# Performance work log

Measured on AMD Instinct MI355X. Metric: run time of the kernel, lower is better.

The kernel has to match this reference:

```python
import jax, jax.numpy as jnp
import numpy as np

N, R, M, E, NE, B = 50000, 500, 120000, 960000, 800000, 8192
D, H1, HID, OC = 200, 256, 512, 50


def setup_inputs() -> dict:
    key = jax.random.key(0)
    ks = jax.random.split(key, 26)
    s = 0.05
    rn = lambda k, shp: jax.random.normal(k, shp, jnp.float32) * s
    return {
        "entity_emb": jax.random.normal(ks[0], (N, D), jnp.float32),
        "rel_emb": jax.random.normal(ks[1], (R, D), jnp.float32),
        "b_x": jax.random.randint(ks[2], (M,), 0, N),
        "b_node_graph_index": jax.random.randint(ks[3], (M,), 0, R),
        "edge_src": jax.random.randint(ks[4], (E,), 0, M),
        "edge_dst": jax.random.randint(ks[5], (E,), 0, M),
        "edge_w": jax.random.uniform(ks[6], (E,), jnp.float32),
        "big_src": jax.random.randint(ks[7], (NE,), 0, N),
        "big_dst": jax.random.randint(ks[8], (NE,), 0, N),
        "big_w": jax.random.uniform(ks[9], (NE,), jnp.float32),
        "perm": jax.random.permutation(ks[10], N),
        "batch_inputs": jnp.stack([
            jax.random.randint(ks[11], (B,), 0, N),
            jax.random.randint(ks[12], (B,), 0, R),
            jax.random.randint(ks[13], (B,), 0, N)], axis=1),
        "W1a": rn(ks[14], (2 * D, H1)), "W1b": rn(ks[15], (H1, D)),
        "W2a": rn(ks[16], (D, H1)), "W2b": rn(ks[17], (H1, D)),
        "Wle": rn(ks[18], (2 * D, 1)), "ble": jnp.zeros((1,), jnp.float32),
        "Wlo": rn(ks[19], (2 * D, D)), "blo": jnp.zeros((D,), jnp.float32),
        "Wg": rn(ks[20], (D, HID)), "Wd": rn(ks[21], (HID, HID)),
        "conv_w": rn(ks[22], (OC, 3)), "conv_b": jnp.zeros((OC,), jnp.float32),
        "fc_w": rn(ks[23], (OC * D, 1)), "fc_b": jnp.zeros((1,), jnp.float32),
    }


def _l2norm(x):
    return x / jnp.maximum(jnp.linalg.norm(x, axis=-1, keepdims=True), 1e-12)


def _gcn(x, src, dst, w, n, Wa, Wb):
    # two-layer GCN over sparse edge list: out = A @ relu(A @ x @ Wa) @ Wb
    agg = lambda h: jax.ops.segment_sum(h[src] * w[:, None], dst, num_segments=n)
    h = jax.nn.relu(agg(x) @ Wa)
    return agg(h) @ Wb


def _seg_softmax(v, idx, n):
    m = jax.ops.segment_max(v, idx, num_segments=n)
    e = jnp.exp(v - m[idx])
    s = jax.ops.segment_sum(e, idx, num_segments=n)
    return e / (s[idx] + 1e-16)


def _mce(ent, rel, b_x, b_gi, src, dst, w, W1a, W1b, Wle, ble, Wlo, blo):
    x = jnp.concatenate([ent[b_x], rel[b_gi]], axis=-1)          # [M, 400]
    e = _gcn(x, src, dst, w, b_x.shape[0], W1a, W1b)             # [M, 200]
    cnt = jax.ops.segment_sum(jnp.ones((b_x.shape[0],), e.dtype), b_x, num_segments=N)
    mean = jax.ops.segment_sum(e, b_x, num_segments=N) / jnp.maximum(cnt, 1.0)[:, None]
    z = mean[b_x]                                                # scatter_mean then gather
    emb = jnp.concatenate([e[b_x], z], axis=-1)                  # [M, 400]
    score = emb @ Wle + ble                                      # [M, 1]
    zs = _seg_softmax(score, b_x, N)                             # segment softmax
    pooled = jax.ops.segment_sum(zs * emb, b_x, num_segments=N)  # [N, 400]
    return (pooled @ Wlo + blo) + ent


def _dgi(h1, h2, Wg, Wd):
    p1 = jax.nn.relu(h1 @ Wg)
    p2 = jax.nn.relu(h2 @ Wg)
    c = jax.nn.sigmoid(jnp.mean(p1, axis=0))                     # readout [HID]
    t = Wd @ c
    return jnp.concatenate([p1 @ t, p2 @ t])                     # [2N]


def _convkb(trip, conv_w, conv_b, fc_w, fc_b):
    # trip [B,3,D]; Conv2d(1, OC, (1,3)) over [B,1,D,3] -> [B,OC,D]
    h = jax.nn.relu(jnp.einsum('bsd,os->bod', trip, conv_w) + conv_b[None, :, None])
    return h.reshape(trip.shape[0], -1) @ fc_w + fc_b            # [B,1]


def reference(entity_emb, rel_emb, b_x, b_node_graph_index, edge_src, edge_dst,
              edge_w, big_src, big_dst, big_w, perm, batch_inputs,
              W1a, W1b, W2a, W2b, Wle, ble, Wlo, blo, Wg, Wd,
              conv_w, conv_b, fc_w, fc_b):
    ent = _l2norm(entity_emb)
    rel = _l2norm(rel_emb)
    ent_shuf = ent[perm]
    ec = _mce(ent, rel, b_x, b_node_graph_index, edge_src, edge_dst, edge_w,
              W1a, W1b, Wle, ble, Wlo, blo)
    ec_ = _mce(ent_shuf, rel, b_x, b_node_graph_index, edge_src, edge_dst, edge_w,
               W1a, W1b, Wle, ble, Wlo, blo)
    eg = _gcn(ec, big_src, big_dst, big_w, N, W2a, W2b)
    eg_ = _gcn(ec_, big_src, big_dst, big_w, N, W2a, W2b)
    local_logits = _dgi(ec, ec_, Wg, Wd)
    global_logits = _dgi(eg, eg_, Wg, Wd)
    trip = jnp.stack([ec[batch_inputs[:, 0]], rel[batch_inputs[:, 1]],
                      ec[batch_inputs[:, 2]]], axis=1)           # [B,3,D]
    out_conv = _convkb(trip, conv_w, conv_b, fc_w, fc_b)
    return out_conv, local_logits, global_logits
```

## Files before the change

kernel.cpp:

```cpp
#include <hip/hip_runtime.h>

#define NN   50000
#define RR   500
#define MM   120000
#define EE   960000
#define NEE  800000
#define BB   8192
#define DD   200
#define HH1  256
#define HIDD 512
#define OCC  50

typedef unsigned int  u32;
typedef unsigned short u16;
typedef __attribute__((ext_vector_type(8))) short bf16x8;
typedef __attribute__((ext_vector_type(4))) float f32x4;

static __device__ __forceinline__ float bf2f(u16 u) {
    u32 x = ((u32)u) << 16;
    return __uint_as_float(x);
}
static __device__ __forceinline__ u16 f2bf(float f) {
    u32 x = __float_as_uint(f);
    u32 r = (x + 0x7FFFu + ((x >> 16) & 1u)) >> 16;
    return (u16)r;
}
static __device__ __forceinline__ u32 pack2(float a, float b) {
    return (u32)f2bf(a) | ((u32)f2bf(b) << 16);
}
static __device__ __forceinline__ void unpack2(u32 v, float& a, float& b) {
    a = bf2f((u16)(v & 0xFFFFu));
    b = bf2f((u16)(v >> 16));
}

static __device__ __forceinline__ float wredsum(float v) {
#pragma unroll
    for (int off = 32; off > 0; off >>= 1) v += __shfl_xor(v, off);
    return v;
}

template<typename T> static __device__ __forceinline__ void stv(T* p, size_t i, float v);
template<> __device__ __forceinline__ void stv<float>(float* p, size_t i, float v) { p[i] = v; }
template<> __device__ __forceinline__ void stv<u16>(u16* p, size_t i, float v) { p[i] = f2bf(v); }

static __device__ __forceinline__ u32 relu2bf(u32 x) {
    if (x & 0x00008000u) x &= 0xFFFF0000u;
    if (x & 0x80000000u) x &= 0x0000FFFFu;
    return x;
}

__global__ void k_l2norm(const float* __restrict__ in, float* __restrict__ outf,
                         u16* __restrict__ outb, int rows) {
    int w = (blockIdx.x * blockDim.x + threadIdx.x) >> 6;
    int lane = threadIdx.x & 63;
    if (w >= rows) return;
    const float* r = in + (size_t)w * DD;
    float s = 0.f;
    for (int d = lane; d < DD; d += 64) { float v = r[d]; s += v * v; }
    s = wredsum(s);
    float inv = 1.0f / fmaxf(sqrtf(s), 1e-12f);
    for (int d = lane; d < DD; d += 64) {
        float v = r[d] * inv;
        if (outf) outf[(size_t)w * DD + d] = v;
        if (outb) outb[(size_t)w * DD + d] = f2bf(v);
    }
}

__global__ void k_gather_perm(const int* __restrict__ bx, const int* __restrict__ perm,
                              int* __restrict__ idx1, int M) {
    int m = blockIdx.x * blockDim.x + threadIdx.x;
    if (m < M) idx1[m] = perm[bx[m]];
}

__global__ void k_edge_idx(const int* __restrict__ srcE, const int* __restrict__ map,
                           int* __restrict__ outE, int n) {
    int e = blockIdx.x * blockDim.x + threadIdx.x;
    if (e < n) outE[e] = map[srcE[e]];
}

__global__ void k_hist(const int* __restrict__ idx, int* __restrict__ cnt, int n) {
    int i = blockIdx.x * blockDim.x + threadIdx.x;
    if (i < n) atomicAdd(&cnt[idx[i]], 1);
}

__global__ __launch_bounds__(1024) void k_scan(const int* __restrict__ in,
                                               int* __restrict__ out, int n) {
    __shared__ int wtot[16];
    __shared__ int wexc[16];
    __shared__ int s_carry;
    int tid = threadIdx.x, lane = tid & 63, wid = tid >> 6;
    if (tid == 0) s_carry = 0;
    __syncthreads();
    for (int base = 0; base < n; base += 1024) {
        int i = base + tid;
        int v = (i < n) ? in[i] : 0;
        int x = v;
#pragma unroll
        for (int off = 1; off < 64; off <<= 1) {
            int t = __shfl_up(x, off);
            if (lane >= off) x += t;
        }
        if (lane == 63) wtot[wid] = x;
        __syncthreads();
        if (wid == 0) {
            int wv2 = (lane < 16) ? wtot[lane] : 0;
            int y = wv2;
#pragma unroll
            for (int off = 1; off < 16; off <<= 1) {
                int t = __shfl_up(y, off);
                if (lane >= off) y += t;
            }
            if (lane < 16) wexc[lane] = y - wv2;
            if (lane == 15) wtot[15] = y;
        }
        __syncthreads();
        if (i < n) out[i] = s_carry + wexc[wid] + (x - v);
        int chunk_total = wtot[15];
        __syncthreads();
        if (tid == 0) s_carry += chunk_total;
        __syncthreads();
    }
    if (threadIdx.x == 0) out[n] = s_carry;
}

__global__ void k_fill2(const int* __restrict__ dst, const int* __restrict__ src,
                        const float* __restrict__ w, int* __restrict__ cursor,
                        int* __restrict__ srcs_out, float* __restrict__ ws_out, int n) {
    int e = blockIdx.x * blockDim.x + threadIdx.x;
    if (e >= n) return;
    int p = atomicAdd(&cursor[dst[e]], 1);
    srcs_out[p] = src[e];
    ws_out[p] = w[e];
}

__global__ void k_fill1(const int* __restrict__ idx, int* __restrict__ cursor,
                        int* __restrict__ outm, int n) {
    int m = blockIdx.x * blockDim.x + threadIdx.x;
    if (m >= n) return;
    int p = atomicAdd(&cursor[idx[m]], 1);
    outm[p] = m;
}

__global__ void k_pull_mce(const int* __restrict__ rp, const int* __restrict__ ivE,
                           const int* __restrict__ giE, const float* __restrict__ wE,
                           const u16* __restrict__ Pent, const u16* __restrict__ Prel,
                           u16* __restrict__ out, int ndst) {
    int wv = (blockIdx.x * blockDim.x + threadIdx.x) >> 6;
    if (wv >= ndst) return;
    int lane = threadIdx.x & 63;
    int beg = rp[wv], end = rp[wv + 1];
    float accA[2] = {0.f, 0.f}, accB[2] = {0.f, 0.f};
    int e = beg;
    for (; e + 4 <= end; e += 4) {
        int i0 = ivE[e], i1 = ivE[e + 1], i2 = ivE[e + 2], i3 = ivE[e + 3];
        int g0 = giE[e], g1 = giE[e + 1], g2 = giE[e + 2], g3 = giE[e + 3];
        float w0 = wE[e], w1 = wE[e + 1], w2 = wE[e + 2], w3 = wE[e + 3];
        const u32* pe0 = (const u32*)(Pent + (size_t)i0 * HH1);
        const u32* pe1 = (const u32*)(Pent + (size_t)i1 * HH1);
        const u32* pe2 = (const u32*)(Pent + (size_t)i2 * HH1);
        const u32* pe3 = (const u32*)(Pent + (size_t)i3 * HH1);
        const u32* pr0 = (const u32*)(Prel + (size_t)g0 * HH1);
        const u32* pr1 = (const u32*)(Prel + (size_t)g1 * HH1);
        const u32* pr2 = (const u32*)(Prel + (size_t)g2 * HH1);
        const u32* pr3 = (const u32*)(Prel + (size_t)g3 * HH1);
        u32 vp[4][2], vr[4][2];
#pragma unroll
        for (int t = 0; t < 2; ++t) {
            int p = lane + 64 * t;
            vp[0][t] = pe0[p]; vp[1][t] = pe1[p]; vp[2][t] = pe2[p]; vp[3][t] = pe3[p];
            vr[0][t] = pr0[p]; vr[1][t] = pr1[p]; vr[2][t] = pr2[p]; vr[3][t] = pr3[p];
        }
#pragma unroll
        for (int t = 0; t < 2; ++t) {
            float a, b, c, d;
            unpack2(vp[0][t], a, b); unpack2(vr[0][t], c, d);
            accA[t] += (a + c) * w0; accB[t] += (b + d) * w0;
            unpack2(vp[1][t], a, b); unpack2(vr[1][t], c, d);
            accA[t] += (a + c) * w1; accB[t] += (b + d) * w1;
            unpack2(vp[2][t], a, b); unpack2(vr[2][t], c, d);
            accA[t] += (a + c) * w2; accB[t] += (b + d) * w2;
            unpack2(vp[3][t], a, b); unpack2(vr[3][t], c, d);
            accA[t] += (a + c) * w3; accB[t] += (b + d) * w3;
        }
    }
    for (; e < end; ++e) {
        int iv = ivE[e], gi = giE[e];
        float w = wE[e];
        const u32* pe = (const u32*)(Pent + (size_t)iv * HH1);
        const u32* pr = (const u32*)(Prel + (size_t)gi * HH1);
#pragma unroll
        for (int t = 0; t < 2; ++t) {
            int p = lane + 64 * t;
            float a, b, c, d;
            unpack2(pe[p], a, b); unpack2(pr[p], c, d);
            accA[t] += (a + c) * w; accB[t] += (b + d) * w;
        }
    }
    u32* o = (u32*)(out + (size_t)wv * HH1);
#pragma unroll
    for (int t = 0; t < 2; ++t) o[lane + 64 * t] = pack2(accA[t], accB[t]);
}

template<int DIMS, typename TIN, typename TOUT>
__global__ void k_pull(const int* __restrict__ rp, const int* __restrict__ srcs,
                       const float* __restrict__ wsrt, const TIN* __restrict__ in,
                       TOUT* __restrict__ out, int ndst) {
    int wv = (blockIdx.x * blockDim.x + threadIdx.x) >> 6;
    if (wv >= ndst) return;
    int lane = threadIdx.x & 63;
    int beg = rp[wv], end = rp[wv + 1];
    constexpr int NP = DIMS / 2;
    constexpr int NT = (NP + 63) / 64;
    float accA[NT], accB[NT];
#pragma unroll
    for (int t = 0; t < NT; ++t) { accA[t] = 0.f; accB[t] = 0.f; }
    int e = beg;
    for (; e + 4 <= end; e += 4) {
        int s0 = srcs[e], s1 = srcs[e + 1], s2 = srcs[e + 2], s3 = srcs[e + 3];
        float w0 = wsrt[e], w1 = wsrt[e + 1], w2 = wsrt[e + 2], w3 = wsrt[e + 3];
        if constexpr (sizeof(TIN) == 2) {
            const u32* r0 = (const u32*)((const u16*)in + (size_t)s0 * DIMS);
            const u32* r1 = (const u32*)((const u16*)in + (size_t)s1 * DIMS);
            const u32* r2 = (const u32*)((const u16*)in + (size_t)s2 * DIMS);
            const u32* r3 = (const u32*)((const u16*)in + (size_t)s3 * DIMS);
            u32 v[4][NT];
#pragma unroll
            for (int t = 0; t < NT; ++t) {
                int p = lane + 64 * t;
                if (p < NP) { v[0][t] = r0[p]; v[1][t] = r1[p]; v[2][t] = r2[p]; v[3][t] = r3[p]; }
            }
#pragma unroll
            for (int t = 0; t < NT; ++t) {
                int p = lane + 64 * t;
                if (p < NP) {
                    float a, b;
                    unpack2(v[0][t], a, b); accA[t] += a * w0; accB[t] += b * w0;
                    unpack2(v[1][t], a, b); accA[t] += a * w1; accB[t] += b * w1;
                    unpack2(v[2][t], a, b); accA[t] += a * w2; accB[t] += b * w2;
                    unpack2(v[3][t], a, b); accA[t] += a * w3; accB[t] += b * w3;
                }
            }
        } else {
            const float2* r0 = (const float2*)((const float*)in + (size_t)s0 * DIMS);
            const float2* r1 = (const float2*)((const float*)in + (size_t)s1 * DIMS);
            const float2* r2 = (const float2*)((const float*)in + (size_t)s2 * DIMS);
            const float2* r3 = (const float2*)((const float*)in + (size_t)s3 * DIMS);
            float2 v[4][NT];
#pragma unroll
            for (int t = 0; t < NT; ++t) {
                int p = lane + 64 * t;
                if (p < NP) { v[0][t] = r0[p]; v[1][t] = r1[p]; v[2][t] = r2[p]; v[3][t] = r3[p]; }
            }
#pragma unroll
            for (int t = 0; t < NT; ++t) {
                int p = lane + 64 * t;
                if (p < NP) {
                    accA[t] += v[0][t].x * w0; accB[t] += v[0][t].y * w0;
                    accA[t] += v[1][t].x * w1; accB[t] += v[1][t].y * w1;
                    accA[t] += v[2][t].x * w2; accB[t] += v[2][t].y * w2;
                    accA[t] += v[3][t].x * w3; accB[t] += v[3][t].y * w3;
                }
            }
        }
    }
    for (; e < end; ++e) {
        int s = srcs[e];
        float w = wsrt[e];
        if constexpr (sizeof(TIN) == 2) {
            const u32* r = (const u32*)((const u16*)in + (size_t)s * DIMS);
#pragma unroll
            for (int t = 0; t < NT; ++t) {
                int p = lane + 64 * t;
                if (p < NP) { float a, b; unpack2(r[p], a, b); accA[t] += a * w; accB[t] += b * w; }
            }
        } else {
            const float2* r = (const float2*)((const float*)in + (size_t)s * DIMS);
#pragma unroll
            for (int t = 0; t < NT; ++t) {
                int p = lane + 64 * t;
                if (p < NP) { float2 v = r[p]; accA[t] += v.x * w; accB[t] += v.y * w; }
            }
        }
    }
    if constexpr (sizeof(TOUT) == 2) {
        u32* o = (u32*)((u16*)out + (size_t)wv * DIMS);
#pragma unroll
        for (int t = 0; t < NT; ++t) {
            int p = lane + 64 * t;
            if (p < NP) o[p] = pack2(accA[t], accB[t]);
        }
    } else {
        float2* o = (float2*)((float*)out + (size_t)wv * DIMS);
#pragma unroll
        for (int t = 0; t < NT; ++t) {
            int p = lane + 64 * t;
            if (p < NP) { float2 v; v.x = accA[t]; v.y = accB[t]; o[p] = v; }
        }
    }
}

__global__ void k_segpool(const int* __restrict__ rpX, const int* __restrict__ mids,
                          const u16* __restrict__ e_buf, u16* __restrict__ pooled, int n) {
    int nv = (blockIdx.x * blockDim.x + threadIdx.x) >> 6;
    if (nv >= n) return;
    int lane = threadIdx.x & 63;
    int beg = rpX[nv], end = rpX[nv + 1];
    int cnt = end - beg;
    float accA[2] = {0.f, 0.f}, accB[2] = {0.f, 0.f};
    int e = beg;
    for (; e + 4 <= end; e += 4) {
        const u32* r0 = (const u32*)(e_buf + (size_t)mids[e] * DD);
        const u32* r1 = (const u32*)(e_buf + (size_t)mids[e + 1] * DD);
        const u32* r2 = (const u32*)(e_buf + (size_t)mids[e + 2] * DD);
        const u32* r3 = (const u32*)(e_buf + (size_t)mids[e + 3] * DD);
        u32 v[4][2];
#pragma unroll
        for (int t = 0; t < 2; ++t) {
            int p = lane + 64 * t;
            if (p < DD / 2) { v[0][t] = r0[p]; v[1][t] = r1[p]; v[2][t] = r2[p]; v[3][t] = r3[p]; }
        }
#pragma unroll
        for (int t = 0; t < 2; ++t) {
            int p = lane + 64 * t;
            if (p < DD / 2) {
                float a, b;
                unpack2(v[0][t], a, b); accA[t] += a; accB[t] += b;
                unpack2(v[1][t], a, b); accA[t] += a; accB[t] += b;
                unpack2(v[2][t], a, b); accA[t] += a; accB[t] += b;
                unpack2(v[3][t], a, b); accA[t] += a; accB[t] += b;
            }
        }
    }
    for (; e < end; ++e) {
        const u32* r = (const u32*)(e_buf + (size_t)mids[e] * DD);
#pragma unroll
        for (int t = 0; t < 2; ++t) {
            int p = lane + 64 * t;
            if (p < DD / 2) { float a, b; unpack2(r[p], a, b); accA[t] += a; accB[t] += b; }
        }
    }
    float inv = 1.0f / fmaxf((float)cnt, 1.0f);
    bool occ = cnt > 0;
    const u32* er = (const u32*)(e_buf + (size_t)nv * DD);
    u32* p0 = (u32*)(pooled + (size_t)nv * (2 * DD));
#pragma unroll
    for (int t = 0; t < 2; ++t) {
        int p = lane + 64 * t;
        if (p < DD / 2) {
            p0[p] = occ ? er[p] : 0u;
            p0[DD / 2 + p] = occ ? pack2(accA[t] * inv, accB[t] * inv) : 0u;
        }
    }
}

template<int AMODE, int RELU_IN, int RELU_OUT, int HAS_BIAS, int HAS_ADD, int FUSE, typename TC>
__global__ __launch_bounds__(256, 2) void k_mfmamm(
    const void* __restrict__ Av, const float* __restrict__ Bw, TC* __restrict__ C,
    int Mr, int Nc, int Kd,
    const float* __restrict__ bias, const u16* __restrict__ addsrc,
    const int* __restrict__ addidx, const float* __restrict__ tvec,
    float* __restrict__ redout) {
    constexpr int BM = 128, BN = 128, BK = 32;
    constexpr int ASTR = 40;
    __shared__ u16 Ahi[BM * ASTR];
    __shared__ u16 Alo[AMODE ? (BM * ASTR) : 8];
    __shared__ u16 Bhi[BN * ASTR];
    __shared__ u16 Blo[BN * ASTR];

    int tid = threadIdx.x;
    int wid = tid >> 6, lane = tid & 63;
    int wr = wid >> 1, wc = wid & 1;
    int r = lane & 15, h = lane >> 4;
    int bm0 = blockIdx.y * BM, bn0 = blockIdx.x * BN;
    int srow = (tid & 15) + 16 * (tid >> 6);
    int sg = (tid >> 4) & 3;

    f32x4 acc[4][4];
#pragma unroll
    for (int i = 0; i < 4; ++i)
#pragma unroll
        for (int j = 0; j < 4; ++j) acc[i][j] = (f32x4){0.f, 0.f, 0.f, 0.f};

    for (int k0 = 0; k0 < Kd; k0 += BK) {
        __syncthreads();
        int kc = k0 + sg * 8;
        bool kok = (kc + 8 <= Kd);
#pragma unroll
        for (int it = 0; it < 2; ++it) {
            int row = srow + 64 * it;
            int gr = bm0 + row;
            u16* dst = Ahi + row * ASTR + sg * 8;
            if (AMODE == 0) {
                const u16* Ab = (const u16*)Av;
                uint4 v = make_uint4(0, 0, 0, 0);
                if (gr < Mr && kok) v = *(const uint4*)(Ab + (size_t)gr * Kd + kc);
                if (RELU_IN) {
                    v.x = relu2bf(v.x); v.y = relu2bf(v.y);
                    v.z = relu2bf(v.z); v.w = relu2bf(v.w);
                }
                *(uint4*)dst = v;
            } else {
                const float* Af = (const float*)Av;
                u32 hw[4] = {0, 0, 0, 0}, lw[4] = {0, 0, 0, 0};
                if (gr < Mr && kok) {
                    const float4* sp = (const float4*)(Af + (size_t)gr * Kd + kc);
                    float4 v0 = sp[0], v1 = sp[1];
                    float vs[8] = {v0.x, v0.y, v0.z, v0.w, v1.x, v1.y, v1.z, v1.w};
#pragma unroll
                    for (int qq = 0; qq < 4; ++qq) {
                        u16 h0 = f2bf(vs[2 * qq]), h1 = f2bf(vs[2 * qq + 1]);
                        hw[qq] = (u32)h0 | ((u32)h1 << 16);
                        u16 l0 = f2bf(vs[2 * qq] - bf2f(h0));
                        u16 l1 = f2bf(vs[2 * qq + 1] - bf2f(h1));
                        lw[qq] = (u32)l0 | ((u32)l1 << 16);
                    }
                }
                *(uint4*)dst = make_uint4(hw[0], hw[1], hw[2], hw[3]);
                *(uint4*)(Alo + row * ASTR + sg * 8) = make_uint4(lw[0], lw[1], lw[2], lw[3]);
            }
        }
#pragma unroll
        for (int it = 0; it < 2; ++it) {
            int n = srow + 64 * it;
            int gn = bn0 + n;
            u32 hw[4] = {0, 0, 0, 0}, lw[4] = {0, 0, 0, 0};
            if (gn < Nc) {
#pragma unroll
                for (int qq = 0; qq < 4; ++qq) {
                    int gk0 = kc + 2 * qq, gk1 = kc + 2 * qq + 1;
                    float b0 = (gk0 < Kd) ? Bw[(size_t)gk0 * Nc + gn] : 0.f;
                    float b1 = (gk1 < Kd) ? Bw[(size_t)gk1 * Nc + gn] : 0.f;
                    u16 h0 = f2bf(b0), h1 = f2bf(b1);
                    hw[qq] = (u32)h0 | ((u32)h1 << 16);
                    u16 l0 = f2bf(b0 - bf2f(h0)), l1 = f2bf(b1 - bf2f(h1));
                    lw[qq] = (u32)l0 | ((u32)l1 << 16);
                }
            }
            *(uint4*)(Bhi + n * ASTR + sg * 8) = make_uint4(hw[0], hw[1], hw[2], hw[3]);
            *(uint4*)(Blo + n * ASTR + sg * 8) = make_uint4(lw[0], lw[1], lw[2], lw[3]);
        }
        __syncthreads();
        bf16x8 af[4], al[4], bh[4], bl[4];
#pragma unroll
        for (int j = 0; j < 4; ++j) {
            int nrow = wc * 64 + j * 16 + r;
            bh[j] = *(const bf16x8*)(Bhi + nrow * ASTR + h * 8);
            bl[j] = *(const bf16x8*)(Blo + nrow * ASTR + h * 8);
        }
#pragma unroll
        for (int i = 0; i < 4; ++i) {
            int mrow = wr * 64 + i * 16 + r;
            af[i] = *(const bf16x8*)(Ahi + mrow * ASTR + h * 8);
            if (AMODE) al[i] = *(const bf16x8*)(Alo + mrow * ASTR + h * 8);
        }
#pragma unroll
        for (int i = 0; i < 4; ++i)
#pragma unroll
            for (int j = 0; j < 4; ++j) {
                acc[i][j] = __builtin_amdgcn_mfma_f32_16x16x32_bf16(af[i], bh[j], acc[i][j], 0, 0, 0);
                acc[i][j] = __builtin_amdgcn_mfma_f32_16x16x32_bf16(af[i], bl[j], acc[i][j], 0, 0, 0);
                if (AMODE)
                    acc[i][j] = __builtin_amdgcn_mfma_f32_16x16x32_bf16(al[i], bh[j], acc[i][j], 0, 0, 0);
            }
    }
    float colacc[4] = {0.f, 0.f, 0.f, 0.f};
#pragma unroll
    for (int i = 0; i < 4; ++i) {
        float rowacc[4] = {0.f, 0.f, 0.f, 0.f};
#pragma unroll
        for (int j = 0; j < 4; ++j) {
            int col = bn0 + wc * 64 + j * 16 + r;
            bool colok = col < Nc;
            float tv = (FUSE == 2 && colok) ? tvec[col] : 0.f;
#pragma unroll
            for (int rg = 0; rg < 4; ++rg) {
                int row = bm0 + wr * 64 + i * 16 + h * 4 + rg;
                float v = acc[i][j][rg];
                if (HAS_BIAS && colok) v += bias[col];
                if (RELU_OUT) v = fmaxf(v, 0.f);
                bool ok = colok && row < Mr;
                if (HAS_ADD && ok) {
                    int r2 = addidx ? addidx[row] : row;
                    v += bf2f(addsrc[(size_t)r2 * Nc + col]);
                }
                if (FUSE != 2 && ok) stv(C, (size_t)row * Nc + col, v);
                if (FUSE == 1 && ok) colacc[j] += v;
                if (FUSE == 2) rowacc[rg] += v * tv;
            }
        }
        if (FUSE == 2) {
#pragma unroll
            for (int rg = 0; rg < 4; ++rg) {
                float val = rowacc[rg];
                val += __shfl_xor(val, 1); val += __shfl_xor(val, 2);
                val += __shfl_xor(val, 4); val += __shfl_xor(val, 8);
                int row = bm0 + wr * 64 + i * 16 + h * 4 + rg;
                if (r == 0 && row < Mr) atomicAdd(&redout[row], val);
            }
        }
    }
    if (FUSE == 1) {
#pragma unroll
        for (int j = 0; j < 4; ++j) {
            float val = colacc[j];
            val += __shfl_xor(val, 16); val += __shfl_xor(val, 32);
            int col = bn0 + wc * 64 + j * 16 + r;
            if (h == 0 && col < Nc) atomicAdd(&redout[col], val);
        }
    }
}

__global__ void k_sigc(const float* __restrict__ csum, float* __restrict__ cvec) {
    int i = threadIdx.x;
    cvec[i] = 1.0f / (1.0f + expf(-csum[i] * (1.0f / (float)NN)));
}

__global__ void k_tmv(const float* __restrict__ Wd, const float* __restrict__ cvec,
                      float* __restrict__ tvec) {
    __shared__ float c[HIDD];
    int lane = threadIdx.x;
    for (int j = lane; j < HIDD; j += 64) c[j] = cvec[j];
    __syncthreads();
    int r0 = blockIdx.x * 16;
    for (int i = r0; i < r0 + 16; ++i) {
        const float* wr = Wd + (size_t)i * HIDD;
        float s = 0.f;
        for (int j = lane; j < HIDD; j += 64) s += wr[j] * c[j];
        s = wredsum(s);
        if (lane == 0) tvec[i] = s;
    }
}

__global__ void k_rowdot512(const float* __restrict__ p, const float* __restrict__ t,
                            float* __restrict__ out, int rows) {
    int g = blockIdx.x * blockDim.x + threadIdx.x;
    int wv = g >> 6;
    if (wv >= rows) return;
    int lane = g & 63;
    const float* r = p + (size_t)wv * HIDD;
    float s = 0.f;
#pragma unroll
    for (int t4 = 0; t4 < 8; ++t4) {
        int d = lane + t4 * 64;
        s += r[d] * t[d];
    }
    s = wredsum(s);
    if (lane == 0) out[wv] = s;
}

__global__ void k_convkb(const u16* __restrict__ ec, const float* __restrict__ rel,
                         const int* __restrict__ bi, const float* __restrict__ cw,
                         const float* __restrict__ cb, const float* __restrict__ fcw,
                         const float* __restrict__ fcb, float* __restrict__ out) {
    __shared__ float t0[DD], t1[DD], t2[DD];
    __shared__ float red[4];
    int b = blockIdx.x, tid = threadIdx.x;
    int i0 = bi[b * 3 + 0], i1 = bi[b * 3 + 1], i2 = bi[b * 3 + 2];
    if (tid < DD) {
        t0[tid] = bf2f(ec[(size_t)i0 * DD + tid]);
        t1[tid] = rel[(size_t)i1 * DD + tid];
        t2[tid] = bf2f(ec[(size_t)i2 * DD + tid]);
    }
    __syncthreads();
    float partial = 0.f;
    if (tid < DD) {
        float a = t0[tid], bb = t1[tid], c = t2[tid];
        for (int o = 0; o < OCC; ++o) {
            float h = fmaxf(cw[o * 3 + 0] * a + cw[o * 3 + 1] * bb + cw[o * 3 + 2] * c + cb[o], 0.f);
            partial += h * fcw[o * DD + tid];
        }
    }
    partial = wredsum(partial);
    if ((tid & 63) == 0) red[tid >> 6] = partial;
    __syncthreads();
    if (tid == 0) out[b] = red[0] + red[1] + red[2] + red[3] + fcb[0];
}

__global__ void k_sentinel(float* out, float val) { out[threadIdx.x] = val; }

extern "C" void kernel_launch(void* const* d_in, const int* in_sizes, int n_in,
                              void* d_out, int out_size, void* d_ws, size_t ws_size,
                              hipStream_t stream) {
    const float* entity_emb = (const float*)d_in[0];
    const float* rel_emb    = (const float*)d_in[1];
    const int*   b_x        = (const int*)d_in[2];
    const int*   b_gi       = (const int*)d_in[3];
    const int*   e_src      = (const int*)d_in[4];
    const int*   e_dst      = (const int*)d_in[5];
    const float* e_w        = (const float*)d_in[6];
    const int*   big_src    = (const int*)d_in[7];
    const int*   big_dst    = (const int*)d_in[8];
    const float* big_w      = (const float*)d_in[9];
    const int*   perm       = (const int*)d_in[10];
    const int*   batch_in   = (const int*)d_in[11];
    const float* W1a        = (const float*)d_in[12];
    const float* W1b        = (const float*)d_in[13];
    const float* W2a        = (const float*)d_in[14];
    const float* W2b        = (const float*)d_in[15];
    const float* Wlo        = (const float*)d_in[18];
    const float* blo        = (const float*)d_in[19];
    const float* Wg         = (const float*)d_in[20];
    const float* Wd         = (const float*)d_in[21];
    const float* conv_w     = (const float*)d_in[22];
    const float* conv_b     = (const float*)d_in[23];
    const float* fc_w       = (const float*)d_in[24];
    const float* fc_b       = (const float*)d_in[25];
    float* out = (float*)d_out;

    size_t off = 0;
    auto balloc = [&](size_t nbytes) {
        size_t p = off;
        off += (nbytes + 511) & ~(size_t)511;
        return p;
    };
    char* base = (char*)d_ws;
    u16*   entb = (u16*)(base + balloc((size_t)NN * DD * 2));
    float* relf = (float*)(base + balloc((size_t)RR * DD * 4));
    u16*   relb = (u16*)(base + balloc((size_t)RR * DD * 2));
    u16*   Pent = (u16*)(base + balloc((size_t)NN * HH1 * 2));
    u16*   Prel = (u16*)(base + balloc((size_t)RR * HH1 * 2));
    int*   idx1 = (int*)(base + balloc((size_t)MM * 4));
    u16*   ecb  = (u16*)(base + balloc((size_t)NN * DD * 2));
    int*   rpB  = (int*)(base + balloc((size_t)(NN + 1) * 4));
    int*   srcB = (int*)(base + balloc((size_t)NEE * 4));
    float* wB   = (float*)(base + balloc((size_t)NEE * 4));
    int*   rpE  = (int*)(base + balloc((size_t)(MM + 1) * 4));
    int*   srcE = (int*)(base + balloc((size_t)EE * 4));
    float* wE   = (float*)(base + balloc((size_t)EE * 4));
    int*   ivE  = (int*)(base + balloc((size_t)EE * 4));
    int*   giE  = (int*)(base + balloc((size_t)EE * 4));
    int*   rpX  = (int*)(base + balloc((size_t)(NN + 1) * 4));
    int*   mids = (int*)(base + balloc((size_t)MM * 4));
    int*   curB = (int*)(base + balloc((size_t)NN * 4));
    int*   curE = (int*)(base + balloc((size_t)MM * 4));
    int*   curX = (int*)(base + balloc((size_t)NN * 4));
    char*  Aarena = base + balloc((size_t)MM * HH1 * 2);
    char*  Barena = base + balloc((size_t)MM * DD * 2);
    char*  Carena = base + balloc((size_t)MM * DD * 2);
    float* csum = (float*)(base + balloc(4 * 2048));
    float* cvec = csum + 512;
    float* t_l  = csum + 1024;
    float* t_g  = csum + 1536;

    if (ws_size < off) {
        k_sentinel<<<dim3(1), dim3(8), 0, stream>>>(out, (float)(ws_size >> 20));
        return;
    }

    u16*   aggx   = (u16*)Aarena;
    u16*   hb     = (u16*)Barena;
    u16*   e_buf  = (u16*)Carena;
    u16*   pooled = (u16*)Aarena;
    float* a1f    = (float*)Aarena;
    float* h2f    = (float*)Barena;
    float* h2bf   = (float*)Aarena;
    float* egf    = (float*)Carena;
    float* pbuf   = (float*)Aarena;

    dim3 blk(256);
    auto wgrid = [](int items) { return dim3((unsigned)((items + 3) / 4)); };
    auto tgrid = [](int items) { return dim3((unsigned)((items + 255) / 256)); };
    auto mmgrid = [](int Mr, int Nc) { return dim3((unsigned)((Nc + 127) / 128), (unsigned)((Mr + 127) / 128)); };

    k_l2norm<<<wgrid(NN), blk, 0, stream>>>(entity_emb, nullptr, entb, NN);
    k_l2norm<<<wgrid(RR), blk, 0, stream>>>(rel_emb, relf, relb, RR);
    k_gather_perm<<<tgrid(MM), blk, 0, stream>>>(b_x, perm, idx1, MM);

    hipMemsetAsync(curB, 0, (size_t)NN * 4, stream);
    hipMemsetAsync(curE, 0, (size_t)MM * 4, stream);
    hipMemsetAsync(curX, 0, (size_t)NN * 4, stream);
    k_hist<<<tgrid(NEE), blk, 0, stream>>>(big_dst, curB, NEE);
    k_hist<<<tgrid(EE), blk, 0, stream>>>(e_dst, curE, EE);
    k_hist<<<tgrid(MM), blk, 0, stream>>>(b_x, curX, MM);
    k_scan<<<dim3(1), dim3(1024), 0, stream>>>(curB, rpB, NN);
    k_scan<<<dim3(1), dim3(1024), 0, stream>>>(curE, rpE, MM);
    k_scan<<<dim3(1), dim3(1024), 0, stream>>>(curX, rpX, NN);
    hipMemcpyAsync(curB, rpB, (size_t)NN * 4, hipMemcpyDeviceToDevice, stream);
    hipMemcpyAsync(curE, rpE, (size_t)MM * 4, hipMemcpyDeviceToDevice, stream);
    hipMemcpyAsync(curX, rpX, (size_t)NN * 4, hipMemcpyDeviceToDevice, stream);
    k_fill2<<<tgrid(NEE), blk, 0, stream>>>(big_dst, big_src, big_w, curB, srcB, wB, NEE);
    k_fill2<<<tgrid(EE), blk, 0, stream>>>(e_dst, e_src, e_w, curE, srcE, wE, EE);
    k_fill1<<<tgrid(MM), blk, 0, stream>>>(b_x, curX, mids, MM);
    k_edge_idx<<<tgrid(EE), blk, 0, stream>>>(srcE, b_gi, giE, EE);

    k_mfmamm<0, 0, 0, 0, 0, 0, u16><<<mmgrid(NN, HH1), blk, 0, stream>>>(
        entb, W1a, Pent, NN, HH1, DD, nullptr, nullptr, nullptr, nullptr, nullptr);
    k_mfmamm<0, 0, 0, 0, 0, 0, u16><<<mmgrid(RR, HH1), blk, 0, stream>>>(
        relb, W1a + (size_t)DD * HH1, Prel, RR, HH1, DD, nullptr, nullptr, nullptr, nullptr, nullptr);

    for (int v = 0; v < 2; ++v) {
        const int* ivmap  = v ? idx1 : b_x;
        const int* addidx = v ? perm : nullptr;

        k_edge_idx<<<tgrid(EE), blk, 0, stream>>>(srcE, ivmap, ivE, EE);
        k_pull_mce<<<wgrid(MM), blk, 0, stream>>>(rpE, ivE, giE, wE, Pent, Prel, aggx, MM);
        k_mfmamm<0, 1, 0, 0, 0, 0, u16><<<mmgrid(MM, DD), blk, 0, stream>>>(
            aggx, W1b, hb, MM, DD, HH1, nullptr, nullptr, nullptr, nullptr, nullptr);
        k_pull<DD, u16, u16><<<wgrid(MM), blk, 0, stream>>>(rpE, srcE, wE, hb, e_buf, MM);
        k_segpool<<<wgrid(NN), blk, 0, stream>>>(rpX, mids, e_buf, pooled, NN);
        k_mfmamm<0, 0, 0, 1, 1, 0, u16><<<mmgrid(NN, DD), blk, 0, stream>>>(
            pooled, Wlo, ecb, NN, DD, 2 * DD, blo, entb, addidx, nullptr, nullptr);

        if (v == 0) {
            hipMemsetAsync(csum, 0, 512 * sizeof(float), stream);
            k_mfmamm<0, 0, 1, 0, 0, 1, float><<<mmgrid(NN, HIDD), blk, 0, stream>>>(
                ecb, Wg, pbuf, NN, HIDD, DD, nullptr, nullptr, nullptr, nullptr, csum);
            k_sigc<<<dim3(1), dim3(512), 0, stream>>>(csum, cvec);
            k_tmv<<<dim3(32), dim3(64), 0, stream>>>(Wd, cvec, t_l);
            k_rowdot512<<<wgrid(NN), blk, 0, stream>>>(pbuf, t_l, out + BB, NN);
            k_convkb<<<dim3(BB), blk, 0, stream>>>(ecb, relf, batch_in,
                                                   conv_w, conv_b, fc_w, fc_b, out);
        } else {
            hipMemsetAsync(out + BB + NN, 0, (size_t)NN * 4, stream);
            k_mfmamm<0, 0, 1, 0, 0, 2, float><<<mmgrid(NN, HIDD), blk, 0, stream>>>(
                ecb, Wg, nullptr, NN, HIDD, DD, nullptr, nullptr, nullptr, t_l, out + BB + NN);
        }

        k_pull<DD, u16, float><<<wgrid(NN), blk, 0, stream>>>(rpB, srcB, wB, ecb, a1f, NN);
        k_mfmamm<1, 0, 1, 0, 0, 0, float><<<mmgrid(NN, HH1), blk, 0, stream>>>(
            a1f, W2a, h2f, NN, HH1, DD, nullptr, nullptr, nullptr, nullptr, nullptr);
        k_mfmamm<1, 0, 0, 0, 0, 0, float><<<mmgrid(NN, DD), blk, 0, stream>>>(
            h2f, W2b, h2bf, NN, DD, HH1, nullptr, nullptr, nullptr, nullptr, nullptr);
        k_pull<DD, float, float><<<wgrid(NN), blk, 0, stream>>>(rpB, srcB, wB, h2bf, egf, NN);

        if (v == 0) {
            hipMemsetAsync(csum, 0, 512 * sizeof(float), stream);
            k_mfmamm<1, 0, 1, 0, 0, 1, float><<<mmgrid(NN, HIDD), blk, 0, stream>>>(
                egf, Wg, pbuf, NN, HIDD, DD, nullptr, nullptr, nullptr, nullptr, csum);
            k_sigc<<<dim3(1), dim3(512), 0, stream>>>(csum, cvec);
            k_tmv<<<dim3(32), dim3(64), 0, stream>>>(Wd, cvec, t_g);
            k_rowdot512<<<wgrid(NN), blk, 0, stream>>>(pbuf, t_g, out + BB + 2 * (size_t)NN, NN);
        } else {
            hipMemsetAsync(out + BB + 3 * (size_t)NN, 0, (size_t)NN * 4, stream);
            k_mfmamm<1, 0, 1, 0, 0, 2, float><<<mmgrid(NN, HIDD), blk, 0, stream>>>(
                egf, Wg, nullptr, NN, HIDD, DD, nullptr, nullptr, nullptr, t_g,
                out + BB + 3 * (size_t)NN);
        }
    }

    (void)in_sizes; (void)n_in; (void)out_size;
}
```

Measured before the change: 2.314 ms.

## Pre-split weights to bf16 hi/lo and store GCN intermediates as bf16 pairs

A new kernel transposes each weight matrix once and splits it into bf16 hi/lo halves. The matmul kernel now reads B fragments for its MFMA operands straight from global memory instead of converting fp32 weights into shared memory on every K tile. The global GCN intermediates, previously fp32, are now stored as hi/lo bf16 pairs that the pull and matmul kernels read directly, which removes the per-tile fp32-to-bf16 split in the A path. This trades repeated conversion work and shared-memory traffic for uncached global B loads per warp and extra prep launches.

Result: no change. 2.324 ms (+0.5%).

```diff
diff --git a/kernel.cpp b/kernel.cpp
--- a/kernel.cpp
+++ b/kernel.cpp
@@ -39,14 +39,16 @@
     return v;
 }
 
-template<typename T> static __device__ __forceinline__ void stv(T* p, size_t i, float v);
-template<> __device__ __forceinline__ void stv<float>(float* p, size_t i, float v) { p[i] = v; }
-template<> __device__ __forceinline__ void stv<u16>(u16* p, size_t i, float v) { p[i] = f2bf(v); }
-
 static __device__ __forceinline__ u32 relu2bf(u32 x) {
     if (x & 0x00008000u) x &= 0xFFFF0000u;
     if (x & 0x80000000u) x &= 0x0000FFFFu;
     return x;
+}
+static __device__ __forceinline__ bf16x8 zero8() {
+    bf16x8 z;
+#pragma unroll
+    for (int i = 0; i < 8; ++i) z[i] = 0;
+    return z;
 }
 
 __global__ void k_l2norm(const float* __restrict__ in, float* __restrict__ outf,
@@ -76,6 +78,17 @@
                            int* __restrict__ outE, int n) {
     int e = blockIdx.x * blockDim.x + threadIdx.x;
     if (e < n) outE[e] = map[srcE[e]];
+}
+
+__global__ void k_prepw(const float* __restrict__ src, int Nc, int Kd,
+                        u16* __restrict__ hi, u16* __restrict__ lo) {
+    int i = blockIdx.x * blockDim.x + threadIdx.x;
+    if (i >= Nc * Kd) return;
+    int n = i / Kd, k = i - n * Kd;
+    float b = src[(size_t)k * Nc + n];
+    u16 hb_ = f2bf(b);
+    hi[i] = hb_;
+    lo[i] = f2bf(b - bf2f(hb_));
 }
 
 __global__ void k_hist(const int* __restrict__ idx, int* __restrict__ cnt, int n) {
@@ -201,10 +214,11 @@
     for (int t = 0; t < 2; ++t) o[lane + 64 * t] = pack2(accA[t], accB[t]);
 }
 
-template<int DIMS, typename TIN, typename TOUT>
+template<int DIMS, int INS, int OUTS>
 __global__ void k_pull(const int* __restrict__ rp, const int* __restrict__ srcs,
-                       const float* __restrict__ wsrt, const TIN* __restrict__ in,
-                       TOUT* __restrict__ out, int ndst) {
+                       const float* __restrict__ wsrt,
+                       const u16* __restrict__ inh, const u16* __restrict__ inl,
+                       u16* __restrict__ outh, u16* __restrict__ outl, int ndst) {
     int wv = (blockIdx.x * blockDim.x + threadIdx.x) >> 6;
     if (wv >= ndst) return;
     int lane = threadIdx.x & 63;
@@ -218,47 +232,42 @@
     for (; e + 4 <= end; e += 4) {
         int s0 = srcs[e], s1 = srcs[e + 1], s2 = srcs[e + 2], s3 = srcs[e + 3];
         float w0 = wsrt[e], w1 = wsrt[e + 1], w2 = wsrt[e + 2], w3 = wsrt[e + 3];
-        if constexpr (sizeof(TIN) == 2) {
-            const u32* r0 = (const u32*)((const u16*)in + (size_t)s0 * DIMS);
-            const u32* r1 = (const u32*)((const u16*)in + (size_t)s1 * DIMS);
-            const u32* r2 = (const u32*)((const u16*)in + (size_t)s2 * DIMS);
-            const u32* r3 = (const u32*)((const u16*)in + (size_t)s3 * DIMS);
-            u32 v[4][NT];
+        const u32* rh[4] = {
+            (const u32*)(inh + (size_t)s0 * DIMS), (const u32*)(inh + (size_t)s1 * DIMS),
+            (const u32*)(inh + (size_t)s2 * DIMS), (const u32*)(inh + (size_t)s3 * DIMS)};
+        u32 vh[4][NT], vl[4][NT];
+#pragma unroll
+        for (int t = 0; t < NT; ++t) {
+            int p = lane + 64 * t;
+            if (p < NP) {
+                vh[0][t] = rh[0][p]; vh[1][t] = rh[1][p];
+                vh[2][t] = rh[2][p]; vh[3][t] = rh[3][p];
+            }
+        }
+        if (INS) {
+            const u32* rl[4] = {
+                (const u32*)(inl + (size_t)s0 * DIMS), (const u32*)(inl + (size_t)s1 * DIMS),
+                (const u32*)(inl + (size_t)s2 * DIMS), (const u32*)(inl + (size_t)s3 * DIMS)};
 #pragma unroll
             for (int t = 0; t < NT; ++t) {
                 int p = lane + 64 * t;
-                if (p < NP) { v[0][t] = r0[p]; v[1][t] = r1[p]; v[2][t] = r2[p]; v[3][t] = r3[p]; }
-            }
+                if (p < NP) {
+                    vl[0][t] = rl[0][p]; vl[1][t] = rl[1][p];
+                    vl[2][t] = rl[2][p]; vl[3][t] = rl[3][p];
+                }
+            }
+        }
+        float ws[4] = {w0, w1, w2, w3};
+#pragma unroll
+        for (int q = 0; q < 4; ++q) {
 #pragma unroll
             for (int t = 0; t < NT; ++t) {
                 int p = lane + 64 * t;
                 if (p < NP) {
                     float a, b;
-                    unpack2(v[0][t], a, b); accA[t] += a * w0; accB[t] += b * w0;
-                    unpack2(v[1][t], a, b); accA[t] += a * w1; accB[t] += b * w1;
-                    unpack2(v[2][t], a, b); accA[t] += a * w2; accB[t] += b * w2;
-                    unpack2(v[3][t], a, b); accA[t] += a * w3; accB[t] += b * w3;
-                }
-            }
-        } else {
-            const float2* r0 = (const float2*)((const float*)in + (size_t)s0 * DIMS);
-            const float2* r1 = (const float2*)((const float*)in + (size_t)s1 * DIMS);
-            const float2* r2 = (const float2*)((const float*)in + (size_t)s2 * DIMS);
-            const float2* r3 = (const float2*)((const float*)in + (size_t)s3 * DIMS);
-            float2 v[4][NT];
-#pragma unroll
-            for (int t = 0; t < NT; ++t) {
-                int p = lane + 64 * t;
-                if (p < NP) { v[0][t] = r0[p]; v[1][t] = r1[p]; v[2][t] = r2[p]; v[3][t] = r3[p]; }
-            }
-#pragma unroll
-            for (int t = 0; t < NT; ++t) {
-                int p = lane + 64 * t;
-                if (p < NP) {
-                    accA[t] += v[0][t].x * w0; accB[t] += v[0][t].y * w0;
-                    accA[t] += v[1][t].x * w1; accB[t] += v[1][t].y * w1;
-                    accA[t] += v[2][t].x * w2; accB[t] += v[2][t].y * w2;
-                    accA[t] += v[3][t].x * w3; accB[t] += v[3][t].y * w3;
+                    unpack2(vh[q][t], a, b);
+                    if (INS) { float a2, b2; unpack2(vl[q][t], a2, b2); a += a2; b += b2; }
+                    accA[t] += a * ws[q]; accB[t] += b * ws[q];
                 }
             }
         }
@@ -266,35 +275,33 @@
     for (; e < end; ++e) {
         int s = srcs[e];
         float w = wsrt[e];
-        if constexpr (sizeof(TIN) == 2) {
-            const u32* r = (const u32*)((const u16*)in + (size_t)s * DIMS);
-#pragma unroll
-            for (int t = 0; t < NT; ++t) {
-                int p = lane + 64 * t;
-                if (p < NP) { float a, b; unpack2(r[p], a, b); accA[t] += a * w; accB[t] += b * w; }
-            }
-        } else {
-            const float2* r = (const float2*)((const float*)in + (size_t)s * DIMS);
-#pragma unroll
-            for (int t = 0; t < NT; ++t) {
-                int p = lane + 64 * t;
-                if (p < NP) { float2 v = r[p]; accA[t] += v.x * w; accB[t] += v.y * w; }
-            }
-        }
-    }
-    if constexpr (sizeof(TOUT) == 2) {
-        u32* o = (u32*)((u16*)out + (size_t)wv * DIMS);
+        const u32* rh = (const u32*)(inh + (size_t)s * DIMS);
+        const u32* rl = INS ? (const u32*)(inl + (size_t)s * DIMS) : nullptr;
 #pragma unroll
         for (int t = 0; t < NT; ++t) {
             int p = lane + 64 * t;
-            if (p < NP) o[p] = pack2(accA[t], accB[t]);
-        }
-    } else {
-        float2* o = (float2*)((float*)out + (size_t)wv * DIMS);
-#pragma unroll
-        for (int t = 0; t < NT; ++t) {
-            int p = lane + 64 * t;
-            if (p < NP) { float2 v; v.x = accA[t]; v.y = accB[t]; o[p] = v; }
+            if (p < NP) {
+                float a, b;
+                unpack2(rh[p], a, b);
+                if (INS) { float a2, b2; unpack2(rl[p], a2, b2); a += a2; b += b2; }
+                accA[t] += a * w; accB[t] += b * w;
+            }
+        }
+    }
+    u32* oh = (u32*)(outh + (size_t)wv * DIMS);
+    u32* ol = OUTS ? (u32*)(outl + (size_t)wv * DIMS) : nullptr;
+#pragma unroll
+    for (int t = 0; t < NT; ++t) {
+        int p = lane + 64 * t;
+        if (p < NP) {
+            if (OUTS == 0) {
+                oh[p] = pack2(accA[t], accB[t]);
+            } else {
+                u16 ha = f2bf(accA[t]), hb_ = f2bf(accB[t]);
+                u16 la = f2bf(accA[t] - bf2f(ha)), lb = f2bf(accB[t] - bf2f(hb_));
+                oh[p] = (u32)ha | ((u32)hb_ << 16);
+                ol[p] = (u32)la | ((u32)lb << 16);
+            }
         }
     }
 }
@@ -353,19 +360,19 @@
     }
 }
 
-template<int AMODE, int RELU_IN, int RELU_OUT, int HAS_BIAS, int HAS_ADD, int FUSE, typename TC>
+template<int AMODE, int RELU_IN, int RELU_OUT, int HAS_BIAS, int HAS_ADD, int FUSE, int CMODE>
 __global__ __launch_bounds__(256, 2) void k_mfmamm(
-    const void* __restrict__ Av, const float* __restrict__ Bw, TC* __restrict__ C,
+    const u16* __restrict__ Ah, const u16* __restrict__ Al,
+    const u16* __restrict__ Bh, const u16* __restrict__ Bl,
+    void* __restrict__ Cv, u16* __restrict__ Cl,
     int Mr, int Nc, int Kd,
     const float* __restrict__ bias, const u16* __restrict__ addsrc,
     const int* __restrict__ addidx, const float* __restrict__ tvec,
     float* __restrict__ redout) {
     constexpr int BM = 128, BN = 128, BK = 32;
     constexpr int ASTR = 40;
-    __shared__ u16 Ahi[BM * ASTR];
-    __shared__ u16 Alo[AMODE ? (BM * ASTR) : 8];
-    __shared__ u16 Bhi[BN * ASTR];
-    __shared__ u16 Blo[BN * ASTR];
+    __shared__ u16 Ahs[BM * ASTR];
+    __shared__ u16 Als[AMODE ? (BM * ASTR) : 8];
 
     int tid = threadIdx.x;
     int wid = tid >> 6, lane = tid & 63;
@@ -389,69 +396,36 @@
         for (int it = 0; it < 2; ++it) {
             int row = srow + 64 * it;
             int gr = bm0 + row;
-            u16* dst = Ahi + row * ASTR + sg * 8;
-            if (AMODE == 0) {
-                const u16* Ab = (const u16*)Av;
-                uint4 v = make_uint4(0, 0, 0, 0);
-                if (gr < Mr && kok) v = *(const uint4*)(Ab + (size_t)gr * Kd + kc);
-                if (RELU_IN) {
-                    v.x = relu2bf(v.x); v.y = relu2bf(v.y);
-                    v.z = relu2bf(v.z); v.w = relu2bf(v.w);
-                }
-                *(uint4*)dst = v;
-            } else {
-                const float* Af = (const float*)Av;
-                u32 hw[4] = {0, 0, 0, 0}, lw[4] = {0, 0, 0, 0};
-                if (gr < Mr && kok) {
-                    const float4* sp = (const float4*)(Af + (size_t)gr * Kd + kc);
-                    float4 v0 = sp[0], v1 = sp[1];
-                    float vs[8] = {v0.x, v0.y, v0.z, v0.w, v1.x, v1.y, v1.z, v1.w};
-#pragma unroll
-                    for (int qq = 0; qq < 4; ++qq) {
-                        u16 h0 = f2bf(vs[2 * qq]), h1 = f2bf(vs[2 * qq + 1]);
-                        hw[qq] = (u32)h0 | ((u32)h1 << 16);
-                        u16 l0 = f2bf(vs[2 * qq] - bf2f(h0));
-                        u16 l1 = f2bf(vs[2 * qq + 1] - bf2f(h1));
-                        lw[qq] = (u32)l0 | ((u32)l1 << 16);
-                    }
-                }
-                *(uint4*)dst = make_uint4(hw[0], hw[1], hw[2], hw[3]);
-                *(uint4*)(Alo + row * ASTR + sg * 8) = make_uint4(lw[0], lw[1], lw[2], lw[3]);
-            }
-        }
-#pragma unroll
-        for (int it = 0; it < 2; ++it) {
-            int n = srow + 64 * it;
-            int gn = bn0 + n;
-            u32 hw[4] = {0, 0, 0, 0}, lw[4] = {0, 0, 0, 0};
-            if (gn < Nc) {
-#pragma unroll
-                for (int qq = 0; qq < 4; ++qq) {
-                    int gk0 = kc + 2 * qq, gk1 = kc + 2 * qq + 1;
-                    float b0 = (gk0 < Kd) ? Bw[(size_t)gk0 * Nc + gn] : 0.f;
-                    float b1 = (gk1 < Kd) ? Bw[(size_t)gk1 * Nc + gn] : 0.f;
-                    u16 h0 = f2bf(b0), h1 = f2bf(b1);
-                    hw[qq] = (u32)h0 | ((u32)h1 << 16);
-                    u16 l0 = f2bf(b0 - bf2f(h0)), l1 = f2bf(b1 - bf2f(h1));
-                    lw[qq] = (u32)l0 | ((u32)l1 << 16);
-                }
-            }
-            *(uint4*)(Bhi + n * ASTR + sg * 8) = make_uint4(hw[0], hw[1], hw[2], hw[3]);
-            *(uint4*)(Blo + n * ASTR + sg * 8) = make_uint4(lw[0], lw[1], lw[2], lw[3]);
+            uint4 v = make_uint4(0, 0, 0, 0), vl = make_uint4(0, 0, 0, 0);
+            if (gr < Mr && kok) {
+                v = *(const uint4*)(Ah + (size_t)gr * Kd + kc);
+                if (AMODE) vl = *(const uint4*)(Al + (size_t)gr * Kd + kc);
+            }
+            if (RELU_IN) {
+                v.x = relu2bf(v.x); v.y = relu2bf(v.y);
+                v.z = relu2bf(v.z); v.w = relu2bf(v.w);
+            }
+            *(uint4*)(Ahs + row * ASTR + sg * 8) = v;
+            if (AMODE) *(uint4*)(Als + row * ASTR + sg * 8) = vl;
         }
         __syncthreads();
-        bf16x8 af[4], al[4], bh[4], bl[4];
+        bf16x8 bh[4], bl[4];
+        int kb = k0 + h * 8;
+        bool kbok = (kb + 8 <= Kd);
 #pragma unroll
         for (int j = 0; j < 4; ++j) {
-            int nrow = wc * 64 + j * 16 + r;
-            bh[j] = *(const bf16x8*)(Bhi + nrow * ASTR + h * 8);
-            bl[j] = *(const bf16x8*)(Blo + nrow * ASTR + h * 8);
-        }
+            int nrow = bn0 + wc * 64 + j * 16 + r;
+            if (nrow < Nc && kbok) {
+                bh[j] = *(const bf16x8*)(Bh + (size_t)nrow * Kd + kb);
+                bl[j] = *(const bf16x8*)(Bl + (size_t)nrow * Kd + kb);
+            } else { bh[j] = zero8(); bl[j] = zero8(); }
+        }
+        bf16x8 af[4], al[4];
 #pragma unroll
         for (int i = 0; i < 4; ++i) {
             int mrow = wr * 64 + i * 16 + r;
-            af[i] = *(const bf16x8*)(Ahi + mrow * ASTR + h * 8);
-            if (AMODE) al[i] = *(const bf16x8*)(Alo + mrow * ASTR + h * 8);
+            af[i] = *(const bf16x8*)(Ahs + mrow * ASTR + h * 8);
+            if (AMODE) al[i] = *(const bf16x8*)(Als + mrow * ASTR + h * 8);
         }
 #pragma unroll
         for (int i = 0; i < 4; ++i)
@@ -483,7 +457,16 @@
                     int r2 = addidx ? addidx[row] : row;
                     v += bf2f(addsrc[(size_t)r2 * Nc + col]);
                 }
-                if (FUSE != 2 && ok) stv(C, (size_t)row * Nc + col, v);
+                if (FUSE != 2 && ok) {
+                    size_t cidx = (size_t)row * Nc + col;
+                    if (CMODE == 0) ((u16*)Cv)[cidx] = f2bf(v);
+                    else if (CMODE == 1) ((float*)Cv)[cidx] = v;
+                    else {
+                        u16 hi_ = f2bf(v);
+                        ((u16*)Cv)[cidx] = hi_;
+                        Cl[cidx] = f2bf(v - bf2f(hi_));
+                    }
+                }
                 if (FUSE == 1 && ok) colacc[j] += v;
                 if (FUSE == 2) rowacc[rg] += v * tv;
             }
@@ -634,6 +617,20 @@
     int*   curB = (int*)(base + balloc((size_t)NN * 4));
     int*   curE = (int*)(base + balloc((size_t)MM * 4));
     int*   curX = (int*)(base + balloc((size_t)NN * 4));
+    u16* w1aT_h  = (u16*)(base + balloc(200 * 256 * 2));
+    u16* w1aT_l  = (u16*)(base + balloc(200 * 256 * 2));
+    u16* w1abT_h = (u16*)(base + balloc(200 * 256 * 2));
+    u16* w1abT_l = (u16*)(base + balloc(200 * 256 * 2));
+    u16* w1bT_h  = (u16*)(base + balloc(256 * 200 * 2));
+    u16* w1bT_l  = (u16*)(base + balloc(256 * 200 * 2));
+    u16* wloT_h  = (u16*)(base + balloc(400 * 200 * 2));
+    u16* wloT_l  = (u16*)(base + balloc(400 * 200 * 2));
+    u16* wgT_h   = (u16*)(base + balloc(200 * 512 * 2));
+    u16* wgT_l   = (u16*)(base + balloc(200 * 512 * 2));
+    u16* w2aT_h  = (u16*)(base + balloc(200 * 256 * 2));
+    u16* w2aT_l  = (u16*)(base + balloc(200 * 256 * 2));
+    u16* w2bT_h  = (u16*)(base + balloc(256 * 200 * 2));
+    u16* w2bT_l  = (u16*)(base + balloc(256 * 200 * 2));
     char*  Aarena = base + balloc((size_t)MM * HH1 * 2);
     char*  Barena = base + balloc((size_t)MM * DD * 2);
     char*  Carena = base + balloc((size_t)MM * DD * 2);
@@ -647,14 +644,19 @@
         return;
     }
 
+    const size_t PL = 20000000;
     u16*   aggx   = (u16*)Aarena;
     u16*   hb     = (u16*)Barena;
     u16*   e_buf  = (u16*)Carena;
     u16*   pooled = (u16*)Aarena;
-    float* a1f    = (float*)Aarena;
-    float* h2f    = (float*)Barena;
-    float* h2bf   = (float*)Aarena;
-    float* egf    = (float*)Carena;
+    u16*   a1h    = (u16*)Aarena;
+    u16*   a1l    = (u16*)(Aarena + PL);
+    u16*   h2h    = (u16*)Barena;
+    u16*   h2l    = (u16*)(Barena + 25600000);
+    u16*   h2bh   = (u16*)Aarena;
+    u16*   h2bl   = (u16*)(Aarena + PL);
+    u16*   egh    = (u16*)Carena;
+    u16*   egl    = (u16*)(Carena + PL);
     float* pbuf   = (float*)Aarena;
 
     dim3 blk(256);
@@ -665,6 +667,13 @@
     k_l2norm<<<wgrid(NN), blk, 0, stream>>>(entity_emb, nullptr, entb, NN);
     k_l2norm<<<wgrid(RR), blk, 0, stream>>>(rel_emb, relf, relb, RR);
     k_gather_perm<<<tgrid(MM), blk, 0, stream>>>(b_x, perm, idx1, MM);
+    k_prepw<<<tgrid(256 * 200), blk, 0, stream>>>(W1a, 256, 200, w1aT_h, w1aT_l);
+    k_prepw<<<tgrid(256 * 200), blk, 0, stream>>>(W1a + 200 * 256, 256, 200, w1abT_h, w1abT_l);
+    k_prepw<<<tgrid(200 * 256), blk, 0, stream>>>(W1b, 200, 256, w1bT_h, w1bT_l);
+    k_prepw<<<tgrid(200 * 400), blk, 0, stream>>>(Wlo, 200, 400, wloT_h, wloT_l);
+    k_prepw<<<tgrid(512 * 200), blk, 0, stream>>>(Wg, 512, 200, wgT_h, wgT_l);
+    k_prepw<<<tgrid(256 * 200), blk, 0, stream>>>(W2a, 256, 200, w2aT_h, w2aT_l);
+    k_prepw<<<tgrid(200 * 256), blk, 0, stream>>>(W2b, 200, 256, w2bT_h, w2bT_l);
 
     hipMemsetAsync(curB, 0, (size_t)NN * 4, stream);
     hipMemsetAsync(curE, 0, (size_t)MM * 4, stream);
@@ -683,10 +692,12 @@
     k_fill1<<<tgrid(MM), blk, 0, stream>>>(b_x, curX, mids, MM);
     k_edge_idx<<<tgrid(EE), blk, 0, stream>>>(srcE, b_gi, giE, EE);
 
-    k_mfmamm<0, 0, 0, 0, 0, 0, u16><<<mmgrid(NN, HH1), blk, 0, stream>>>(
-        entb, W1a, Pent, NN, HH1, DD, nullptr, nullptr, nullptr, nullptr, nullptr);
-    k_mfmamm<0, 0, 0, 0, 0, 0, u16><<<mmgrid(RR, HH1), blk, 0, stream>>>(
-        relb, W1a + (size_t)DD * HH1, Prel, RR, HH1, DD, nullptr, nullptr, nullptr, nullptr, nullptr);
+    k_mfmamm<0, 0, 0, 0, 0, 0, 0><<<mmgrid(NN, HH1), blk, 0, stream>>>(
+        entb, nullptr, w1aT_h, w1aT_l, Pent, nullptr, NN, HH1, DD,
+        nullptr, nullptr, nullptr, nullptr, nullptr);
+    k_mfmamm<0, 0, 0, 0, 0, 0, 0><<<mmgrid(RR, HH1), blk, 0, stream>>>(
+        relb, nullptr, w1abT_h, w1abT_l, Prel, nullptr, RR, HH1, DD,
+        nullptr, nullptr, nullptr, nullptr, nullptr);
 
     for (int v = 0; v < 2; ++v) {
         const int* ivmap  = v ? idx1 : b_x;
@@ -694,17 +705,21 @@
 
         k_edge_idx<<<tgrid(EE), blk, 0, stream>>>(srcE, ivmap, ivE, EE);
         k_pull_mce<<<wgrid(MM), blk, 0, stream>>>(rpE, ivE, giE, wE, Pent, Prel, aggx, MM);
-        k_mfmamm<0, 1, 0, 0, 0, 0, u16><<<mmgrid(MM, DD), blk, 0, stream>>>(
-            aggx, W1b, hb, MM, DD, HH1, nullptr, nullptr, nullptr, nullptr, nullptr);
-        k_pull<DD, u16, u16><<<wgrid(MM), blk, 0, stream>>>(rpE, srcE, wE, hb, e_buf, MM);
+        k_mfmamm<0, 1, 0, 0, 0, 0, 0><<<mmgrid(MM, DD), blk, 0, stream>>>(
+            aggx, nullptr, w1bT_h, w1bT_l, hb, nullptr, MM, DD, HH1,
+            nullptr, nullptr, nullptr, nullptr, nullptr);
+        k_pull<DD, 0, 0><<<wgrid(MM), blk, 0, stream>>>(rpE, srcE, wE, hb, nullptr,
+                                                        e_buf, nullptr, MM);
         k_segpool<<<wgrid(NN), blk, 0, stream>>>(rpX, mids, e_buf, pooled, NN);
-        k_mfmamm<0, 0, 0, 1, 1, 0, u16><<<mmgrid(NN, DD), blk, 0, stream>>>(
-            pooled, Wlo, ecb, NN, DD, 2 * DD, blo, entb, addidx, nullptr, nullptr);
+        k_mfmamm<0, 0, 0, 1, 1, 0, 0><<<mmgrid(NN, DD), blk, 0, stream>>>(
+            pooled, nullptr, wloT_h, wloT_l, ecb, nullptr, NN, DD, 2 * DD,
+            blo, entb, addidx, nullptr, nullptr);
 
         if (v == 0) {
             hipMemsetAsync(csum, 0, 512 * sizeof(float), stream);
-            k_mfmamm<0, 0, 1, 0, 0, 1, float><<<mmgrid(NN, HIDD), blk, 0, stream>>>(
-                ecb, Wg, pbuf, NN, HIDD, DD, nullptr, nullptr, nullptr, nullptr, csum);
+            k_mfmamm<0, 0, 1, 0, 0, 1, 1><<<mmgrid(NN, HIDD), blk, 0, stream>>>(
+                ecb, nullptr, wgT_h, wgT_l, pbuf, nullptr, NN, HIDD, DD,
+                nullptr, nullptr, nullptr, nullptr, csum);
             k_sigc<<<dim3(1), dim3(512), 0, stream>>>(csum, cvec);
             k_tmv<<<dim3(32), dim3(64), 0, stream>>>(Wd, cvec, t_l);
             k_rowdot512<<<wgrid(NN), blk, 0, stream>>>(pbuf, t_l, out + BB, NN);
@@ -712,29 +727,35 @@
                                                    conv_w, conv_b, fc_w, fc_b, out);
         } else {
             hipMemsetAsync(out + BB + NN, 0, (size_t)NN * 4, stream);
-            k_mfmamm<0, 0, 1, 0, 0, 2, float><<<mmgrid(NN, HIDD), blk, 0, stream>>>(
-                ecb, Wg, nullptr, NN, HIDD, DD, nullptr, nullptr, nullptr, t_l, out + BB + NN);
-        }
-
-        k_pull<DD, u16, float><<<wgrid(NN), blk, 0, stream>>>(rpB, srcB, wB, ecb, a1f, NN);
-        k_mfmamm<1, 0, 1, 0, 0, 0, float><<<mmgrid(NN, HH1), blk, 0, stream>>>(
-            a1f, W2a, h2f, NN, HH1, DD, nullptr, nullptr, nullptr, nullptr, nullptr);
-        k_mfmamm<1, 0, 0, 0, 0, 0, float><<<mmgrid(NN, DD), blk, 0, stream>>>(
-            h2f, W2b, h2bf, NN, DD, HH1, nullptr, nullptr, nullptr, nullptr, nullptr);
-        k_pull<DD, float, float><<<wgrid(NN), blk, 0, stream>>>(rpB, srcB, wB, h2bf, egf, NN);
+            k_mfmamm<0, 0, 1, 0, 0, 2, 1><<<mmgrid(NN, HIDD), blk, 0, stream>>>(
+                ecb, nullptr, wgT_h, wgT_l, nullptr, nullptr, NN, HIDD, DD,
+                nullptr, nullptr, nullptr, t_l, out + BB + NN);
+        }
+
+        k_pull<DD, 0, 1><<<wgrid(NN), blk, 0, stream>>>(rpB, srcB, wB, ecb, nullptr,
+                                                        a1h, a1l, NN);
+        k_mfmamm<1, 0, 1, 0, 0, 0, 2><<<mmgrid(NN, HH1), blk, 0, stream>>>(
+            a1h, a1l, w2aT_h, w2aT_l, h2h, h2l, NN, HH1, DD,
+            nullptr, nullptr, nullptr, nullptr, nullptr);
+        k_mfmamm<1, 0, 0, 0, 0, 0, 2><<<mmgrid(NN, DD), blk, 0, stream>>>(
+            h2h, h2l, w2bT_h, w2bT_l, h2bh, h2bl, NN, DD, HH1,
+            nullptr, nullptr, nullptr, nullptr, nullptr);
+        k_pull<DD, 1, 1><<<wgrid(NN), blk, 0, stream>>>(rpB, srcB, wB, h2bh, h2bl,
+                                                        egh, egl, NN);
 
         if (v == 0) {
             hipMemsetAsync(csum, 0, 512 * sizeof(float), stream);
-            k_mfmamm<1, 0, 1, 0, 0, 1, float><<<mmgrid(NN, HIDD), blk, 0, stream>>>(
-                egf, Wg, pbuf, NN, HIDD, DD, nullptr, nullptr, nullptr, nullptr, csum);
+            k_mfmamm<1, 0, 1, 0, 0, 1, 1><<<mmgrid(NN, HIDD), blk, 0, stream>>>(
+                egh, egl, wgT_h, wgT_l, pbuf, nullptr, NN, HIDD, DD,
+                nullptr, nullptr, nullptr, nullptr, csum);
             k_sigc<<<dim3(1), dim3(512), 0, stream>>>(csum, cvec);
             k_tmv<<<dim3(32), dim3(64), 0, stream>>>(Wd, cvec, t_g);
             k_rowdot512<<<wgrid(NN), blk, 0, stream>>>(pbuf, t_g, out + BB + 2 * (size_t)NN, NN);
         } else {
             hipMemsetAsync(out + BB + 3 * (size_t)NN, 0, (size_t)NN * 4, stream);
-            k_mfmamm<1, 0, 1, 0, 0, 2, float><<<mmgrid(NN, HIDD), blk, 0, stream>>>(
-                egf, Wg, nullptr, NN, HIDD, DD, nullptr, nullptr, nullptr, t_g,
-                out + BB + 3 * (size_t)NN);
+            k_mfmamm<1, 0, 1, 0, 0, 2, 1><<<mmgrid(NN, HIDD), blk, 0, stream>>>(
+                egh, egl, wgT_h, wgT_l, nullptr, nullptr, NN, HIDD, DD,
+                nullptr, nullptr, nullptr, t_g, out + BB + 3 * (size_t)NN);
         }
     }
 
```
